# Kernel tuning notes

Hardware: AMD Instinct MI355X
Metric: run time of the kernel (lower is better)

Reference implementation:

```python
import jax, jax.numpy as jnp
import numpy as np

H, DK, DV = 16, 64, 64

def setup_inputs() -> dict:
    key = jax.random.key(0)
    ks = jax.random.split(key, 5)
    S, E = 2048, 1024
    return {
        "x": jax.random.normal(ks[0], (S, E), jnp.float32),
        "Wq": jax.random.normal(ks[1], (H * DK, E), jnp.float32) * 0.02,
        "Wk": jax.random.normal(ks[2], (H * DK, E), jnp.float32) * 0.02,
        "Wv": jax.random.normal(ks[3], (H * DV, E), jnp.float32) * 0.02,
        "Wo": jax.random.normal(ks[4], (H * DV, H * DV), jnp.float32) * 0.02,
    }

def reference(x, Wq, Wk, Wv, Wo):
    S = x.shape[0]
    # Fused QKV projections (equivalent to per-head Linear with concatenated weights)
    Q = (x @ Wq.T).reshape(S, H, DK).transpose(1, 0, 2)  # [H,S,dk]
    K = (x @ Wk.T).reshape(S, H, DK).transpose(1, 0, 2)  # [H,S,dk]
    V = (x @ Wv.T).reshape(S, H, DV).transpose(1, 0, 2)  # [H,S,dv]
    scale = 1.0 / np.sqrt(DK).astype(np.float32)
    scores = jnp.einsum('hsd,htd->hst', Q, K) * scale    # [H,S,S]
    weights = jax.nn.softmax(scores, axis=-1)
    A = jnp.einsum('hst,htv->hsv', weights, V)           # [H,S,dv]
    A1 = A.transpose(1, 0, 2).reshape(S, H * DV)         # concat heads on last dim
    return A1 @ Wo.T
```

## Files before the change

### kernel.cpp

```cpp
#include <hip/hip_runtime.h>
#include <hip/hip_bf16.h>
#include <stdint.h>

typedef uint16_t u16;
typedef uint32_t u32;
typedef float    f32x4  __attribute__((ext_vector_type(4)));
typedef __bf16   bf16x8 __attribute__((ext_vector_type(8)));
typedef uint16_t u16x8  __attribute__((ext_vector_type(8)));
typedef uint16_t u16x4  __attribute__((ext_vector_type(4)));
typedef uint32_t u32x4  __attribute__((ext_vector_type(4)));

#define HH 16
#define SS 2048
#define EE 1024
#define DD 64

__device__ inline u16 f2bf(float f) {
  uint32_t u = __builtin_bit_cast(uint32_t, f);
  u += 0x7fff + ((u >> 16) & 1);
  return (u16)(u >> 16);
}
__device__ inline float bf2f(u16 b) {
  return __builtin_bit_cast(float, (uint32_t)b << 16);
}

__device__ inline u32 cvtpk(float lo, float hi) {
  u32 r;
  asm("v_cvt_pk_bf16_f32 %0, %1, %2" : "=v"(r) : "v"(lo), "v"(hi));
  return r;
}

__device__ inline void gload_lds16(const void* g, void* l) {
  __builtin_amdgcn_global_load_lds(
      (const __attribute__((address_space(1))) uint32_t*)g,
      (__attribute__((address_space(3))) uint32_t*)l, 16, 0, 0);
}

__global__ __launch_bounds__(256) void convert_kernel(
    const float* __restrict__ x,  const float* __restrict__ wq,
    const float* __restrict__ wk, const float* __restrict__ wv,
    const float* __restrict__ wo,
    u16* __restrict__ xb, u16* __restrict__ wqkvb, u16* __restrict__ wob) {
  const int64_t M1 = 1024 * 1024;
  int64_t e = ((int64_t)blockIdx.x * 256 + threadIdx.x) * 4;
  const float* src; u16* dst; int64_t off;
  if (e < 2 * M1)      { src = x;  dst = xb;           off = e; }
  else if (e < 3 * M1) { src = wq; dst = wqkvb;        off = e - 2 * M1; }
  else if (e < 4 * M1) { src = wk; dst = wqkvb + M1;   off = e - 3 * M1; }
  else if (e < 5 * M1) { src = wv; dst = wqkvb + 2*M1; off = e - 4 * M1; }
  else                 { src = wo; dst = wob;          off = e - 5 * M1; }
  float4 v = *(const float4*)(src + off);
  u16x4 o;
  o[0] = f2bf(v.x); o[1] = f2bf(v.y); o[2] = f2bf(v.z); o[3] = f2bf(v.w);
  *(u16x4*)(dst + off) = o;
}

template <int EPI, int K, int N>
__global__ __launch_bounds__(256, 4) void gemm_kernel(
    const u16* __restrict__ A, const u16* __restrict__ B,
    u16* __restrict__ q_ws, u16* __restrict__ k_ws, u16* __restrict__ vt_ws,
    float* __restrict__ Cout) {
  constexpr int BM = 64, BN = 128, BK = 64;
  __shared__ __align__(16) u16 As[BM * BK];
  __shared__ __align__(16) u16 Bs[BN * BK];
  const int t = threadIdx.x;
  const int lane = t & 63, w = t >> 6;
  const int wr = w >> 1, wc = w & 1;
  const int fr = lane & 15, fg = lane >> 4;

  const int nwg = gridDim.x * gridDim.y;
  const int bid = blockIdx.y * gridDim.x + blockIdx.x;
  const int swz = (bid & 7) * (nwg >> 3) + (bid >> 3);
  const int m0 = (swz / gridDim.x) * BM, n0 = (swz % gridDim.x) * BN;

  f32x4 acc[2][4] = {};

  for (int k0 = 0; k0 < K; k0 += BK) {
#pragma unroll
    for (int it = 0; it < 2; ++it) {
      const int c = t + it * 256, row = c >> 3, sch = (c & 7) ^ (row & 7);
      gload_lds16(A + (int64_t)(m0 + row) * K + k0 + sch * 8,
                  As + (c & ~63) * 8);
    }
#pragma unroll
    for (int it = 0; it < 4; ++it) {
      const int c = t + it * 256, row = c >> 3, sch = (c & 7) ^ (row & 7);
      gload_lds16(B + (int64_t)(n0 + row) * K + k0 + sch * 8,
                  Bs + (c & ~63) * 8);
    }
    __syncthreads();
    bf16x8 af[2][2], bfr[4][2];
#pragma unroll
    for (int mi = 0; mi < 2; ++mi)
#pragma unroll
      for (int kc = 0; kc < 2; ++kc) {
        const int row = wr * 32 + mi * 16 + fr;
        const int cc = (kc * 4 + fg) ^ (row & 7);
        af[mi][kc] = __builtin_bit_cast(bf16x8, *(const u16x8*)&As[row * 64 + cc * 8]);
      }
#pragma unroll
    for (int ni = 0; ni < 4; ++ni)
#pragma unroll
      for (int kc = 0; kc < 2; ++kc) {
        const int row = wc * 64 + ni * 16 + fr;
        const int cc = (kc * 4 + fg) ^ (row & 7);
        bfr[ni][kc] = __builtin_bit_cast(bf16x8, *(const u16x8*)&Bs[row * 64 + cc * 8]);
      }
#pragma unroll
    for (int kc = 0; kc < 2; ++kc)
#pragma unroll
      for (int mi = 0; mi < 2; ++mi)
#pragma unroll
        for (int ni = 0; ni < 4; ++ni)
          acc[mi][ni] = __builtin_amdgcn_mfma_f32_16x16x32_bf16(
              af[mi][kc], bfr[ni][kc], acc[mi][ni], 0, 0, 0);
    __syncthreads();
  }

#pragma unroll
  for (int mi = 0; mi < 2; ++mi)
#pragma unroll
    for (int ni = 0; ni < 4; ++ni)
#pragma unroll
      for (int r = 0; r < 4; ++r) {
        const int m = m0 + wr * 32 + mi * 16 + fg * 4 + r;
        const int n = n0 + wc * 64 + ni * 16 + fr;
        const float v = acc[mi][ni][r];
        if constexpr (EPI == 0) {
          const int which = n >> 10, nn = n & 1023, h = nn >> 6, d = nn & 63;
          const u16 bv = f2bf(v);
          if (which == 0)      q_ws[((int64_t)h * SS + m) * DD + d] = bv;
          else if (which == 1) k_ws[((int64_t)h * SS + m) * DD + d] = bv;
          else                 vt_ws[((int64_t)h * DD + d) * SS + m] = bv;
        } else {
          Cout[(int64_t)m * N + n] = v;
        }
      }
}

__global__ __launch_bounds__(256, 5) void attn_kernel(
    const u16* __restrict__ q_ws, const u16* __restrict__ k_ws,
    const u16* __restrict__ vt_ws, u16* __restrict__ opart,
    float* __restrict__ lsum) {
  constexpr int NTS = SS / 64 / 2;
  __shared__ __align__(16) u16 lds[16384];
  const int t = threadIdx.x;
  const int lane = t & 63, w = t >> 6;
  const int ql = lane & 15, g = lane >> 4;
  const int h = blockIdx.y, qb = blockIdx.x, sp = blockIdx.z;
  const int kt0 = sp * NTS;
  const int qbase = qb * 64 + w * 16;

  const u16* Qh = q_ws + ((int64_t)h * SS + qbase) * DD;
  const u16* Kh = k_ws + ((int64_t)h * SS + kt0 * 64) * DD;
  const u16* Vh = vt_ws + (int64_t)h * DD * SS + kt0 * 64;

  const int r0 = t >> 3, ch = t & 7, r1 = (t + 256) >> 3;
  const int sch0 = ch ^ (r0 & 7), sch1 = ch ^ (r1 & 7);
  const int64_t ko0 = (int64_t)r0 * DD + sch0 * 8;
  const int64_t ko1 = (int64_t)r1 * DD + sch1 * 8;
  const int64_t vo0 = (int64_t)r0 * SS + sch0 * 8;
  const int64_t vo1 = (int64_t)r1 * SS + sch1 * 8;
  const int dst0 = (t & ~63) * 8, dst1 = dst0 + 2048;

  bf16x8 qf[2];
#pragma unroll
  for (int dd = 0; dd < 2; ++dd)
    qf[dd] = __builtin_bit_cast(
        bf16x8, *(const u16x8*)(Qh + ql * DD + dd * 32 + g * 8));

  f32x4 o[4] = {};
  float l_run = 0.f;
  const float C2 = 0.18033688f;

  auto qk = [&](f32x4 (&s)[4], const int kb_) {
    __builtin_amdgcn_s_setprio(1);
#pragma unroll
    for (int kb = 0; kb < 4; ++kb) {
      const int key = kb * 16 + ql;
      f32x4 z = {};
#pragma unroll
      for (int dd = 0; dd < 2; ++dd) {
        bf16x8 kf = __builtin_bit_cast(
            bf16x8,
            *(const u16x8*)&lds[kb_ * 4096 + key * 64 +
                                (((dd * 4 + g) ^ (ql & 7)) * 8)]);
        z = __builtin_amdgcn_mfma_f32_16x16x32_bf16(kf, qf[dd], z, 0, 0, 0);
      }
      s[kb] = z;
    }
    __builtin_amdgcn_s_setprio(0);
  };

  auto smpv = [&](f32x4 (&s)[4], const int vb_) {
#pragma unroll
    for (int kb = 0; kb < 4; ++kb)
#pragma unroll
      for (int r = 0; r < 4; ++r) {
        const float pv = exp2f(s[kb][r] * C2);
        s[kb][r] = pv;
        l_run += pv;
      }
#pragma unroll
    for (int ks = 0; ks < 2; ++ks) {
      u32 x0 = cvtpk(s[2 * ks][0], s[2 * ks][1]);
      u32 x1 = cvtpk(s[2 * ks][2], s[2 * ks][3]);
      u32 y0 = cvtpk(s[2 * ks + 1][0], s[2 * ks + 1][1]);
      u32 y1 = cvtpk(s[2 * ks + 1][2], s[2 * ks + 1][3]);
      asm("v_permlane32_swap_b32 %0, %1" : "+v"(x0), "+v"(y0));
      asm("v_permlane16_swap_b32 %0, %1" : "+v"(x0), "+v"(y0));
      asm("v_permlane32_swap_b32 %0, %1" : "+v"(x1), "+v"(y1));
      asm("v_permlane16_swap_b32 %0, %1" : "+v"(x1), "+v"(y1));
      u32x4 aw; aw[0] = x0; aw[1] = x1; aw[2] = y0; aw[3] = y1;
      const bf16x8 pa = __builtin_bit_cast(bf16x8, aw);
      __builtin_amdgcn_s_setprio(1);
#pragma unroll
      for (int nb = 0; nb < 4; ++nb) {
        const int dv = nb * 16 + ql;
        bf16x8 vf = __builtin_bit_cast(
            bf16x8,
            *(const u16x8*)&lds[8192 + vb_ * 4096 + dv * 64 +
                                (((ks * 4 + g) ^ (ql & 7)) * 8)]);
        o[nb] = __builtin_amdgcn_mfma_f32_16x16x32_bf16(pa, vf, o[nb], 0, 0, 0);
      }
      __builtin_amdgcn_s_setprio(0);
    }
  };

  gload_lds16(Kh + ko0, lds + dst0);
  gload_lds16(Kh + ko1, lds + dst1);

  f32x4 sA[4], sB[4];
#pragma unroll
  for (int tt = 0; tt < NTS; ++tt) {
    __syncthreads();
    if (tt + 1 < NTS) {
      const u16* Kn = Kh + (int64_t)(tt + 1) * 64 * DD;
      const int kb = ((tt + 1) & 1) * 4096;
      gload_lds16(Kn + ko0, lds + kb + dst0);
      gload_lds16(Kn + ko1, lds + kb + dst1);
    }
    {
      const u16* Vn = Vh + tt * 64;
      const int vb = 8192 + (tt & 1) * 4096;
      gload_lds16(Vn + vo0, lds + vb + dst0);
      gload_lds16(Vn + vo1, lds + vb + dst1);
    }
    if (tt & 1) {
      qk(sB, tt & 1);
      smpv(sA, (tt - 1) & 1);
    } else {
      qk(sA, tt & 1);
      if (tt > 0) smpv(sB, (tt - 1) & 1);
    }
  }
  __syncthreads();
  smpv(sB, (NTS - 1) & 1);

  float l = l_run;
  l += __shfl_xor(l, 16);
  l += __shfl_xor(l, 32);
  const int64_t rowbase = ((int64_t)sp * HH + h) * SS;
#pragma unroll
  for (int r = 0; r < 4; ++r) {
    const int q = qbase + g * 4 + r;
#pragma unroll
    for (int nb = 0; nb < 4; ++nb)
      opart[(rowbase + q) * DD + nb * 16 + ql] = f2bf(o[nb][r]);
  }
  if (g == 0) lsum[rowbase + qbase + ql] = l;
}

__global__ __launch_bounds__(256) void combine_kernel(
    const u16* __restrict__ opart, const float* __restrict__ lsum,
    u16* __restrict__ a_ws) {
  const int rid = blockIdx.x * 4 + (threadIdx.x >> 6);
  const int lane = threadIdx.x & 63;
  const int h = rid >> 11, q = rid & 2047;
  const float inv = 1.0f / (lsum[rid] + lsum[HH * SS + rid]);
  const float o1 = bf2f(opart[(int64_t)rid * DD + lane]);
  const float o2 = bf2f(opart[((int64_t)HH * SS + rid) * DD + lane]);
  a_ws[(int64_t)q * (HH * DD) + h * DD + lane] = f2bf((o1 + o2) * inv);
}

extern "C" void kernel_launch(void* const* d_in, const int* in_sizes, int n_in,
                              void* d_out, int out_size, void* d_ws, size_t ws_size,
                              hipStream_t stream) {
  const float* x  = (const float*)d_in[0];
  const float* wq = (const float*)d_in[1];
  const float* wk = (const float*)d_in[2];
  const float* wv = (const float*)d_in[3];
  const float* wo = (const float*)d_in[4];
  char* ws = (char*)d_ws;
  const int64_t Mi = 1 << 20;
  u16* xb    = (u16*)(ws + 0 * Mi);
  u16* wqkv  = (u16*)(ws + 4 * Mi);
  u16* wob   = (u16*)(ws + 10 * Mi);
  u16* q_ws  = (u16*)(ws + 12 * Mi);
  u16* k_ws  = (u16*)(ws + 16 * Mi);
  u16* vt    = (u16*)(ws + 20 * Mi);
  u16*   opart = (u16*)(ws + 0 * Mi);
  float* lsv   = (float*)(ws + 8 * Mi);
  u16* a_ws  = (u16*)(ws + 12 * Mi);
  float* out = (float*)d_out;

  convert_kernel<<<6144, 256, 0, stream>>>(x, wq, wk, wv, wo, xb, wqkv, wob);

  gemm_kernel<0, 1024, 3072><<<dim3(3072 / 128, 2048 / 64), 256, 0, stream>>>(
      xb, wqkv, q_ws, k_ws, vt, nullptr);

  attn_kernel<<<dim3(SS / 64, HH, 2), 256, 0, stream>>>(
      q_ws, k_ws, vt, opart, lsv);

  combine_kernel<<<HH * SS / 4, 256, 0, stream>>>(opart, lsv, a_ws);

  gemm_kernel<1, 1024, 1024><<<dim3(1024 / 128, 2048 / 64), 256, 0, stream>>>(
      a_ws, wob, nullptr, nullptr, nullptr, out);
}
```

Measured before the change: 86.56 us.

## Fold softmax scale into Q, compute row sums via MFMA, shrink output GEMM tile

The scale constant is folded into Q in the QKV GEMM epilogue, so the attention kernel computes exp2 directly without a per-element multiply. The scalar row-sum accumulation and cross-lane shuffles are replaced by an extra MFMA against a ones vector, which yields the row sums in accumulator layout. The output projection GEMM uses BN=64 to double its grid for better CU occupancy. The risks are an extra MFMA per block, sums taken from bf16-rounded probabilities, and Q rounded to bf16 after scaling.

After: 82.83 us. -4.3%, faster.

```diff
diff --git a/kernel.cpp b/kernel.cpp
--- a/kernel.cpp
+++ b/kernel.cpp
@@ -55,12 +55,14 @@
   *(u16x4*)(dst + off) = o;
 }
 
-template <int EPI, int K, int N>
+template <int EPI, int K, int N, int BN>
 __global__ __launch_bounds__(256, 4) void gemm_kernel(
     const u16* __restrict__ A, const u16* __restrict__ B,
     u16* __restrict__ q_ws, u16* __restrict__ k_ws, u16* __restrict__ vt_ws,
     float* __restrict__ Cout) {
-  constexpr int BM = 64, BN = 128, BK = 64;
+  constexpr int BM = 64, BK = 64;
+  constexpr int NFB = BN / 32;
+  constexpr float C2 = 0.18033688f;
   __shared__ __align__(16) u16 As[BM * BK];
   __shared__ __align__(16) u16 Bs[BN * BK];
   const int t = threadIdx.x;
@@ -73,7 +75,7 @@
   const int swz = (bid & 7) * (nwg >> 3) + (bid >> 3);
   const int m0 = (swz / gridDim.x) * BM, n0 = (swz % gridDim.x) * BN;
 
-  f32x4 acc[2][4] = {};
+  f32x4 acc[2][NFB] = {};
 
   for (int k0 = 0; k0 < K; k0 += BK) {
 #pragma unroll
@@ -83,13 +85,13 @@
                   As + (c & ~63) * 8);
     }
 #pragma unroll
-    for (int it = 0; it < 4; ++it) {
+    for (int it = 0; it < BN * 8 / 256; ++it) {
       const int c = t + it * 256, row = c >> 3, sch = (c & 7) ^ (row & 7);
       gload_lds16(B + (int64_t)(n0 + row) * K + k0 + sch * 8,
                   Bs + (c & ~63) * 8);
     }
     __syncthreads();
-    bf16x8 af[2][2], bfr[4][2];
+    bf16x8 af[2][2], bfr[NFB][2];
 #pragma unroll
     for (int mi = 0; mi < 2; ++mi)
 #pragma unroll
@@ -99,10 +101,10 @@
         af[mi][kc] = __builtin_bit_cast(bf16x8, *(const u16x8*)&As[row * 64 + cc * 8]);
       }
 #pragma unroll
-    for (int ni = 0; ni < 4; ++ni)
+    for (int ni = 0; ni < NFB; ++ni)
 #pragma unroll
       for (int kc = 0; kc < 2; ++kc) {
-        const int row = wc * 64 + ni * 16 + fr;
+        const int row = wc * (BN / 2) + ni * 16 + fr;
         const int cc = (kc * 4 + fg) ^ (row & 7);
         bfr[ni][kc] = __builtin_bit_cast(bf16x8, *(const u16x8*)&Bs[row * 64 + cc * 8]);
       }
@@ -111,7 +113,7 @@
 #pragma unroll
       for (int mi = 0; mi < 2; ++mi)
 #pragma unroll
-        for (int ni = 0; ni < 4; ++ni)
+        for (int ni = 0; ni < NFB; ++ni)
           acc[mi][ni] = __builtin_amdgcn_mfma_f32_16x16x32_bf16(
               af[mi][kc], bfr[ni][kc], acc[mi][ni], 0, 0, 0);
     __syncthreads();
@@ -120,18 +122,20 @@
 #pragma unroll
   for (int mi = 0; mi < 2; ++mi)
 #pragma unroll
-    for (int ni = 0; ni < 4; ++ni)
+    for (int ni = 0; ni < NFB; ++ni)
 #pragma unroll
       for (int r = 0; r < 4; ++r) {
         const int m = m0 + wr * 32 + mi * 16 + fg * 4 + r;
-        const int n = n0 + wc * 64 + ni * 16 + fr;
+        const int n = n0 + wc * (BN / 2) + ni * 16 + fr;
         const float v = acc[mi][ni][r];
         if constexpr (EPI == 0) {
           const int which = n >> 10, nn = n & 1023, h = nn >> 6, d = nn & 63;
-          const u16 bv = f2bf(v);
-          if (which == 0)      q_ws[((int64_t)h * SS + m) * DD + d] = bv;
-          else if (which == 1) k_ws[((int64_t)h * SS + m) * DD + d] = bv;
-          else                 vt_ws[((int64_t)h * DD + d) * SS + m] = bv;
+          if (which == 0)
+            q_ws[((int64_t)h * SS + m) * DD + d] = f2bf(v * C2);
+          else if (which == 1)
+            k_ws[((int64_t)h * SS + m) * DD + d] = f2bf(v);
+          else
+            vt_ws[((int64_t)h * DD + d) * SS + m] = f2bf(v);
         } else {
           Cout[(int64_t)m * N + n] = v;
         }
@@ -169,9 +173,13 @@
     qf[dd] = __builtin_bit_cast(
         bf16x8, *(const u16x8*)(Qh + ql * DD + dd * 32 + g * 8));
 
+  u16x8 ov;
+#pragma unroll
+  for (int j = 0; j < 8; ++j) ov[j] = 0x3F80;
+  const bf16x8 onesf = __builtin_bit_cast(bf16x8, ov);
+
   f32x4 o[4] = {};
-  float l_run = 0.f;
-  const float C2 = 0.18033688f;
+  f32x4 o_l = {};
 
   auto qk = [&](f32x4 (&s)[4], const int kb_) {
     __builtin_amdgcn_s_setprio(1);
@@ -196,11 +204,8 @@
 #pragma unroll
     for (int kb = 0; kb < 4; ++kb)
 #pragma unroll
-      for (int r = 0; r < 4; ++r) {
-        const float pv = exp2f(s[kb][r] * C2);
-        s[kb][r] = pv;
-        l_run += pv;
-      }
+      for (int r = 0; r < 4; ++r)
+        s[kb][r] = exp2f(s[kb][r]);
 #pragma unroll
     for (int ks = 0; ks < 2; ++ks) {
       u32 x0 = cvtpk(s[2 * ks][0], s[2 * ks][1]);
@@ -214,6 +219,7 @@
       u32x4 aw; aw[0] = x0; aw[1] = x1; aw[2] = y0; aw[3] = y1;
       const bf16x8 pa = __builtin_bit_cast(bf16x8, aw);
       __builtin_amdgcn_s_setprio(1);
+      o_l = __builtin_amdgcn_mfma_f32_16x16x32_bf16(pa, onesf, o_l, 0, 0, 0);
 #pragma unroll
       for (int nb = 0; nb < 4; ++nb) {
         const int dv = nb * 16 + ql;
@@ -257,9 +263,6 @@
   __syncthreads();
   smpv(sB, (NTS - 1) & 1);
 
-  float l = l_run;
-  l += __shfl_xor(l, 16);
-  l += __shfl_xor(l, 32);
   const int64_t rowbase = ((int64_t)sp * HH + h) * SS;
 #pragma unroll
   for (int r = 0; r < 4; ++r) {
@@ -268,7 +271,11 @@
     for (int nb = 0; nb < 4; ++nb)
       opart[(rowbase + q) * DD + nb * 16 + ql] = f2bf(o[nb][r]);
   }
-  if (g == 0) lsum[rowbase + qbase + ql] = l;
+  if (ql == 0) {
+#pragma unroll
+    for (int r = 0; r < 4; ++r)
+      lsum[rowbase + qbase + g * 4 + r] = o_l[r];
+  }
 }
 
 __global__ __launch_bounds__(256) void combine_kernel(
@@ -306,7 +313,7 @@
 
   convert_kernel<<<6144, 256, 0, stream>>>(x, wq, wk, wv, wo, xb, wqkv, wob);
 
-  gemm_kernel<0, 1024, 3072><<<dim3(3072 / 128, 2048 / 64), 256, 0, stream>>>(
+  gemm_kernel<0, 1024, 3072, 128><<<dim3(3072 / 128, 2048 / 64), 256, 0, stream>>>(
       xb, wqkv, q_ws, k_ws, vt, nullptr);
 
   attn_kernel<<<dim3(SS / 64, HH, 2), 256, 0, stream>>>(
@@ -314,6 +321,6 @@
 
   combine_kernel<<<HH * SS / 4, 256, 0, stream>>>(opart, lsv, a_ws);
 
-  gemm_kernel<1, 1024, 1024><<<dim3(1024 / 128, 2048 / 64), 256, 0, stream>>>(
+  gemm_kernel<1, 1024, 1024, 64><<<dim3(1024 / 64, 2048 / 64), 256, 0, stream>>>(
       a_ws, wob, nullptr, nullptr, nullptr, out);
 }
```
